# Performance work log

Measured on AMD Instinct MI355X. Metric: run time of the kernel, lower is better.

Reference implementation:

```python
import jax, jax.numpy as jnp
import numpy as np

CH = 256
GROUPS = 8
EPS = 1e-5


def setup_inputs() -> dict:
    key = jax.random.key(0)
    ks = jax.random.split(key, 12)
    b, c, h, w = 8, CH, 64, 64
    s = 0.02
    return {
        "x": jax.random.normal(ks[0], (b, c, h, w), dtype=jnp.float32),
        "gn_w": jnp.ones((c,), dtype=jnp.float32),
        "gn_b": jnp.zeros((c,), dtype=jnp.float32),
        "wq": jax.random.normal(ks[1], (c, c), dtype=jnp.float32) * s,
        "bq": jax.random.normal(ks[2], (c,), dtype=jnp.float32) * s,
        "wk": jax.random.normal(ks[3], (c, c), dtype=jnp.float32) * s,
        "bk": jax.random.normal(ks[4], (c,), dtype=jnp.float32) * s,
        "wv": jax.random.normal(ks[5], (c, c), dtype=jnp.float32) * s,
        "bv": jax.random.normal(ks[6], (c,), dtype=jnp.float32) * s,
        "wp": jax.random.normal(ks[7], (c, c), dtype=jnp.float32) * s,
        "bp": jax.random.normal(ks[8], (c,), dtype=jnp.float32) * s,
    }


def reference(x, gn_w, gn_b, wq, bq, wk, bk, wv, bv, wp, bp):
    b, c, h, w = x.shape
    n = h * w
    # GroupNorm(8, c): normalize over (c//g, h, w) per group, then affine per-channel
    xg = x.reshape(b, GROUPS, c // GROUPS, n)
    mu = xg.mean(axis=(2, 3), keepdims=True)
    var = xg.var(axis=(2, 3), keepdims=True)
    y = ((xg - mu) * jax.lax.rsqrt(var + EPS)).reshape(b, c, n)
    y = y * gn_w[None, :, None] + gn_b[None, :, None]
    # 1x1 convs == channel matmuls
    q = jnp.einsum('oc,bcn->bno', wq, y) + bq              # [b, n, c]
    k = jnp.einsum('oc,bcn->bon', wk, y) + bk[:, None]     # [b, c, n]
    v = jnp.einsum('oc,bcn->bno', wv, y) + bv              # [b, n, c]
    scale = 1.0 / jnp.sqrt(jnp.float32(c))
    attn = jax.nn.softmax(jnp.einsum('bnc,bcm->bnm', q, k) * scale, axis=-1)  # [b, n, n]
    out = jnp.einsum('bnm,bmc->bcn', attn, v)              # [b, c, n]
    proj = jnp.einsum('oc,bcn->bon', wp, out) + bp[:, None]
    return x + proj.reshape(b, c, h, w)
```

## Files before the change

### kernel.cpp

```cpp
#include <hip/hip_runtime.h>

typedef __attribute__((ext_vector_type(8))) short s16x8;
typedef __attribute__((ext_vector_type(4))) float f32x4;
typedef __attribute__((ext_vector_type(16))) float f32x16;
typedef __attribute__((ext_vector_type(4))) uint u32x4;
typedef __attribute__((ext_vector_type(2))) uint u32x2;
typedef __attribute__((ext_vector_type(2))) long s64x2;
typedef __attribute__((ext_vector_type(8))) int i32x8;
typedef unsigned char u8;

#define MFMA16(a, b, c) __builtin_amdgcn_mfma_f32_16x16x32_bf16((a), (b), (c), 0, 0, 0)
#define MFMAF8(a, b, c) __builtin_amdgcn_mfma_f32_32x32x16_fp8_fp8((a), (b), (c), 0, 0, 0)
#define MFMAMX(a, b, c) \
  __builtin_amdgcn_mfma_scale_f32_32x32x64_f8f6f4((a), (b), (c), 0, 0, 0, 0x7F7F7F7F, 0, 0x7F7F7F7F)

__device__ __forceinline__ ushort f2bf(float f) {
  uint u = __builtin_bit_cast(uint, f);
  u = (u + 0x7fffu + ((u >> 16) & 1u)) >> 16;
  return (ushort)u;
}
__device__ __forceinline__ float max3f(float a, float b, float c) {
  return fmaxf(fmaxf(a, b), c);
}

__global__ __launch_bounds__(256) void cvt_w_kernel(
    const float* __restrict__ s0, const float* __restrict__ s1,
    const float* __restrict__ s2, const float* __restrict__ s3,
    ushort* __restrict__ d0, ushort* __restrict__ d1,
    ushort* __restrict__ d2, ushort* __restrict__ d3,
    const float* __restrict__ bq, const float* __restrict__ bk,
    const float* __restrict__ bv, float* __restrict__ bcat) {
  int i = blockIdx.x * 256 + threadIdx.x;
  const float4* s[4] = {(const float4*)s0, (const float4*)s1, (const float4*)s2, (const float4*)s3};
  ushort* d[4] = {d0, d1, d2, d3};
#pragma unroll
  for (int m = 0; m < 4; ++m) {
    float4 v = s[m][i];
    uint lo = (uint)f2bf(v.x) | ((uint)f2bf(v.y) << 16);
    uint hi = (uint)f2bf(v.z) | ((uint)f2bf(v.w) << 16);
    *(uint2*)(d[m] + (size_t)i * 4) = make_uint2(lo, hi);
  }
  if (blockIdx.x == 0) {
    int t = threadIdx.x;
    bcat[t] = bq[t];
    bcat[256 + t] = bk[t];
    bcat[512 + t] = bv[t];
  }
}

__global__ __launch_bounds__(256) void gn_stats_kernel(
    const float* __restrict__ x, float2* __restrict__ partial) {
  int bid = blockIdx.x;
  int b = bid >> 6, g = (bid >> 3) & 7, sl = bid & 7;
  const float4* src = (const float4*)(x + ((size_t)b * 256 + g * 32) * 4096) + sl * 4096;
  float s = 0.f, ss = 0.f;
#pragma unroll 4
  for (int i = threadIdx.x; i < 4096; i += 256) {
    float4 v = src[i];
    s += v.x + v.y + v.z + v.w;
    ss += v.x * v.x + v.y * v.y + v.z * v.z + v.w * v.w;
  }
#pragma unroll
  for (int off = 32; off; off >>= 1) {
    s += __shfl_down(s, off);
    ss += __shfl_down(ss, off);
  }
  __shared__ float ps[4], pss[4];
  int w = threadIdx.x >> 6, lane = threadIdx.x & 63;
  if (lane == 0) { ps[w] = s; pss[w] = ss; }
  __syncthreads();
  if (threadIdx.x == 0) {
    float2 r;
    r.x = ps[0] + ps[1] + ps[2] + ps[3];
    r.y = pss[0] + pss[1] + pss[2] + pss[3];
    partial[bid] = r;
  }
}

__global__ __launch_bounds__(256) void gn_apply_kernel(
    const float* __restrict__ x, const float2* __restrict__ partial,
    const float* __restrict__ gw, const float* __restrict__ gb,
    ushort* __restrict__ y) {
  int bid = blockIdx.x;
  int b = bid >> 8;
  int rem = bid & 255;
  int ct = rem >> 6, nt = rem & 63;
  int t = threadIdx.x;
  __shared__ float xs[64][65];
  __shared__ float smu2[2], srs2[2];
  if (t < 2) {
    float S = 0.f, SS = 0.f;
#pragma unroll
    for (int i = 0; i < 8; ++i) {
      float2 p = partial[(b << 6) | ((2 * ct + t) << 3) | i];
      S += p.x;
      SS += p.y;
    }
    float mu = S * (1.f / 131072.f);
    float var = SS * (1.f / 131072.f) - mu * mu;
    smu2[t] = mu;
    srs2[t] = rsqrtf(var + 1e-5f);
  }
  const float* xb = x + ((size_t)b * 256 + ct * 64) * 4096 + nt * 64;
  {
    int r = t >> 2, q = t & 3;
    const float4* src = (const float4*)(xb + (size_t)r * 4096 + q * 16);
#pragma unroll
    for (int i = 0; i < 4; ++i) {
      float4 v = src[i];
      xs[r][q * 16 + i * 4 + 0] = v.x;
      xs[r][q * 16 + i * 4 + 1] = v.y;
      xs[r][q * 16 + i * 4 + 2] = v.z;
      xs[r][q * 16 + i * 4 + 3] = v.w;
    }
  }
  __syncthreads();
  {
    int nr = t >> 2, q = t & 3;
    int c0 = q * 16;
    ushort tmp[16];
#pragma unroll
    for (int i = 0; i < 16; ++i) {
      int ci = c0 + i;
      int ch = ct * 64 + ci;
      int gsel = ci >> 5;
      float sc = gw[ch] * srs2[gsel];
      float sh = gb[ch] - smu2[gsel] * sc;
      float v = xs[ci][nr] * sc + sh;
      tmp[i] = f2bf(v);
    }
    ushort* dst = y + ((size_t)b * 4096 + nt * 64 + nr) * 256 + ct * 64 + c0;
    uint p[8];
#pragma unroll
    for (int j = 0; j < 8; ++j) p[j] = (uint)tmp[2 * j] | ((uint)tmp[2 * j + 1] << 16);
    *(uint4*)dst = make_uint4(p[0], p[1], p[2], p[3]);
    *((uint4*)dst + 1) = make_uint4(p[4], p[5], p[6], p[7]);
  }
}

template <int MODE>
__global__ __launch_bounds__(256) void gemm_bt(
    const ushort* __restrict__ A, const ushort* __restrict__ B,
    size_t aB, size_t bB, int M, int N,
    const float* __restrict__ bias, const float* __restrict__ resid,
    size_t rB, void* __restrict__ Cout, size_t cB) {
  int mTiles = M >> 7;
  int tm = blockIdx.x % mTiles, tn = blockIdx.x / mTiles;
  const ushort* Ab = A + blockIdx.y * aB + (size_t)tm * 128 * 256;
  const ushort* Bb = B + blockIdx.y * bB + (size_t)tn * 128 * 256;

  __shared__ ushort As[2][8192];
  __shared__ ushort Bs[2][8192];

  int t = threadIdx.x, lane = t & 63, w = t >> 6;
  int wr = w >> 1, wc = w & 1, lq = lane & 15, lg = lane >> 4;

  f32x4 acc[4][4];
#pragma unroll
  for (int i = 0; i < 4; ++i)
#pragma unroll
    for (int j = 0; j < 4; ++j) acc[i][j] = f32x4{0.f, 0.f, 0.f, 0.f};

  auto stageT = [&](int kb, int db) {
#pragma unroll
    for (int i = 0; i < 4; ++i) {
      int bu = i * 256 + w * 64;
      int u = bu + lane;
      int row = u >> 3, c = u & 7;
      int cl = c ^ (row & 7);
      const ushort* sa = Ab + (size_t)row * 256 + kb * 64 + cl * 8;
      __builtin_amdgcn_global_load_lds(
          (const __attribute__((address_space(1))) uint*)sa,
          (__attribute__((address_space(3))) uint*)(&As[db][0] + bu * 8), 16, 0, 0);
      const ushort* sb = Bb + (size_t)row * 256 + kb * 64 + cl * 8;
      __builtin_amdgcn_global_load_lds(
          (const __attribute__((address_space(1))) uint*)sb,
          (__attribute__((address_space(3))) uint*)(&Bs[db][0] + bu * 8), 16, 0, 0);
    }
  };

  stageT(0, 0);

#pragma unroll 1
  for (int kb = 0; kb < 4; ++kb) {
    if (kb < 3) {
      stageT(kb + 1, (kb + 1) & 1);
      asm volatile("s_waitcnt vmcnt(8)" ::: "memory");
    } else {
      asm volatile("s_waitcnt vmcnt(0)" ::: "memory");
    }
    __builtin_amdgcn_s_barrier();
    const ushort* Abf = &As[kb & 1][0];
    const ushort* Bbf = &Bs[kb & 1][0];
#pragma unroll
    for (int ks = 0; ks < 2; ++ks) {
      s16x8 af[4], bf[4];
#pragma unroll
      for (int mt = 0; mt < 4; ++mt) {
        int row = wr * 64 + mt * 16 + lq;
        af[mt] = *(const s16x8*)&Abf[row * 64 + (((ks * 4 + lg) ^ (row & 7)) << 3)];
      }
#pragma unroll
      for (int nt = 0; nt < 4; ++nt) {
        int row = wc * 64 + nt * 16 + lq;
        bf[nt] = *(const s16x8*)&Bbf[row * 64 + (((ks * 4 + lg) ^ (row & 7)) << 3)];
      }
#pragma unroll
      for (int mt = 0; mt < 4; ++mt)
#pragma unroll
        for (int nt = 0; nt < 4; ++nt)
          acc[mt][nt] = MFMA16(af[mt], bf[nt], acc[mt][nt]);
    }
    asm volatile("" ::: "memory");
    __builtin_amdgcn_s_barrier();
    asm volatile("" ::: "memory");
  }

  int mBase = tm * 128 + wr * 64;
  int nBase = tn * 128 + wc * 64;
#pragma unroll
  for (int mt = 0; mt < 4; ++mt) {
#pragma unroll
    for (int nt = 0; nt < 4; ++nt) {
#pragma unroll
      for (int r = 0; r < 4; ++r) {
        int row = mBase + mt * 16 + lg * 4 + r;
        int col = nBase + nt * 16 + lq;
        float v = acc[mt][nt][r];
        if (MODE == 6) {
          v += bias[col];
          uint pk8 = (uint)__builtin_amdgcn_cvt_pk_fp8_f32(v, v, 0, false);
          u8* Cb = (u8*)Cout + blockIdx.y * cB;
          if (col < 512) {
            u8* C = Cb + ((col >= 256) ? 16777216 : 0);
            C[(size_t)row * 256 + (col & 255)] = (u8)(pk8 & 0xff);
          } else {
            int rr = row & 31;
            int pr = (row & ~31) |
                     ((rr & 7) | (((rr >> 4) & 1) << 3) | (((rr >> 3) & 1) << 4));
            u8* C = Cb + 33554432;
            C[(size_t)(col - 512) * 4096 + pr] = (u8)(pk8 & 0xff);
          }
        } else {
          v += bias[row];
          size_t idx = (size_t)row * N + col;
          float* C = (float*)Cout + blockIdx.y * cB;
          C[idx] = v + resid[blockIdx.y * rB + idx];
        }
      }
    }
  }
}

__global__ __launch_bounds__(256) void gemm_proj_kernel(
    const ushort* __restrict__ A, const ushort* __restrict__ P0,
    const ushort* __restrict__ P1, const float* __restrict__ mlb,
    const float* __restrict__ bias, const float* __restrict__ resid,
    float* __restrict__ Cout) {
  const size_t MAT = 4096 * 256;
  int tm = blockIdx.x & 1, tn = blockIdx.x >> 1;
  int bb = blockIdx.y;
  const ushort* Ab = A + (size_t)tm * 128 * 256;
  const ushort* P0b = P0 + (size_t)bb * MAT + (size_t)tn * 128 * 256;
  const ushort* P1b = P1 + (size_t)bb * MAT + (size_t)tn * 128 * 256;
  const int mlbase = bb * 4096 + tn * 128;

  __shared__ ushort As[2][8192];
  __shared__ ushort Bs[2][8192];

  int t = threadIdx.x, lane = t & 63, w = t >> 6;
  int wr = w >> 1, wc = w & 1, lq = lane & 15, lg = lane >> 4;

  f32x4 acc[4][4];
#pragma unroll
  for (int i = 0; i < 4; ++i)
#pragma unroll
    for (int j = 0; j < 4; ++j) acc[i][j] = f32x4{0.f, 0.f, 0.f, 0.f};

  u32x4 rb0[4], rb1[4];
  float rw0[4], rw1[4];

  auto issueA = [&](int kb, int db) {
#pragma unroll
    for (int i = 0; i < 4; ++i) {
      int bu = i * 256 + w * 64;
      int u = bu + lane;
      int row = u >> 3, c = u & 7;
      int cl = c ^ (row & 7);
      const ushort* sa = Ab + (size_t)row * 256 + kb * 64 + cl * 8;
      __builtin_amdgcn_global_load_lds(
          (const __attribute__((address_space(1))) uint*)sa,
          (__attribute__((address_space(3))) uint*)(&As[db][0] + bu * 8), 16, 0, 0);
    }
  };
  auto loadB = [&](int kb) {
#pragma unroll
    for (int i = 0; i < 4; ++i) {
      int bu = i * 256 + w * 64;
      int u = bu + lane;
      int row = u >> 3, c = u & 7;
      int cl = c ^ (row & 7);
      rb0[i] = *(const u32x4*)(P0b + (size_t)row * 256 + kb * 64 + cl * 8);
      rb1[i] = *(const u32x4*)(P1b + (size_t)row * 256 + kb * 64 + cl * 8);
      int gr = mlbase + row;
      float m0 = mlb[gr], m1 = mlb[32768 + gr];
      float l0 = mlb[65536 + gr], l1 = mlb[98304 + gr];
      float M = fmaxf(m0, m1);
      float e0 = __builtin_exp2f(m0 - M), e1 = __builtin_exp2f(m1 - M);
      float inv = 1.f / (l0 * e0 + l1 * e1);
      rw0[i] = e0 * inv;
      rw1[i] = e1 * inv;
    }
  };
  auto writeB = [&](int db) {
#pragma unroll
    for (int i = 0; i < 4; ++i) {
      int bu = i * 256 + w * 64;
      uint outw[4];
#pragma unroll
      for (int j = 0; j < 4; ++j) {
        float alo = __builtin_bit_cast(float, rb0[i][j] << 16);
        float ahi = __builtin_bit_cast(float, rb0[i][j] & 0xffff0000u);
        float blo = __builtin_bit_cast(float, rb1[i][j] << 16);
        float bhi = __builtin_bit_cast(float, rb1[i][j] & 0xffff0000u);
        float flo = alo * rw0[i] + blo * rw1[i];
        float fhi = ahi * rw0[i] + bhi * rw1[i];
        asm("v_cvt_pk_bf16_f32 %0, %1, %2" : "=v"(outw[j]) : "v"(flo), "v"(fhi));
      }
      u32x4 ov = {outw[0], outw[1], outw[2], outw[3]};
      *(u32x4*)&Bs[db][(size_t)(bu + lane) * 8] = ov;
    }
  };

  issueA(0, 0);
  loadB(0);
  writeB(0);
  asm volatile("s_waitcnt vmcnt(0) lgkmcnt(0)" ::: "memory");
  __builtin_amdgcn_s_barrier();

#pragma unroll
  for (int kb = 0; kb < 4; ++kb) {
    const int db = kb & 1;
    if (kb < 3) {
      issueA(kb + 1, db ^ 1);
      loadB(kb + 1);
    }
    const ushort* Abf = &As[db][0];
    const ushort* Bbf = &Bs[db][0];
#pragma unroll
    for (int ks = 0; ks < 2; ++ks) {
      s16x8 af[4], bf[4];
#pragma unroll
      for (int mt = 0; mt < 4; ++mt) {
        int row = wr * 64 + mt * 16 + lq;
        af[mt] = *(const s16x8*)&Abf[row * 64 + (((ks * 4 + lg) ^ (row & 7)) << 3)];
      }
#pragma unroll
      for (int nt = 0; nt < 4; ++nt) {
        int row = wc * 64 + nt * 16 + lq;
        bf[nt] = *(const s16x8*)&Bbf[row * 64 + (((ks * 4 + lg) ^ (row & 7)) << 3)];
      }
#pragma unroll
      for (int mt = 0; mt < 4; ++mt)
#pragma unroll
        for (int nt = 0; nt < 4; ++nt)
          acc[mt][nt] = MFMA16(af[mt], bf[nt], acc[mt][nt]);
    }
    if (kb < 3) writeB(db ^ 1);
    asm volatile("s_waitcnt vmcnt(0) lgkmcnt(0)" ::: "memory");
    __builtin_amdgcn_s_barrier();
  }

  int mBase = tm * 128 + wr * 64;
  int nBase = tn * 128 + wc * 64;
#pragma unroll
  for (int mt = 0; mt < 4; ++mt) {
#pragma unroll
    for (int nt = 0; nt < 4; ++nt) {
#pragma unroll
      for (int r = 0; r < 4; ++r) {
        int row = mBase + mt * 16 + lg * 4 + r;
        int col = nBase + nt * 16 + lq;
        size_t idx = (size_t)bb * MAT + (size_t)row * 4096 + col;
        Cout[idx] = acc[mt][nt][r] + bias[row] + resid[idx];
      }
    }
  }
}

__global__ __launch_bounds__(256, 2) void attn11_kernel(
    const u8* __restrict__ q, const u8* __restrict__ k,
    const u8* __restrict__ vT, ushort* __restrict__ pb0,
    ushort* __restrict__ pb1, float* __restrict__ mlbuf) {
  const int bb = blockIdx.x & 7;
  const int rem = blockIdx.x >> 3;
  const int qt = rem & 31;
  const int half = rem >> 5;
  const int t = threadIdx.x, w = t >> 6, lane = t & 63;
  const int lq = lane & 31, lh = lane >> 5;

  __shared__ u8 Lf[65536];

  const u8* kb = k + (size_t)bb * (4096 * 256);
  const u8* vb = vT + (size_t)bb * (4096 * 256);

  const int qrow = bb * 4096 + qt * 128 + w * 32 + lq;
  i32x8 qf8[4];
  {
    const u8* qp = q + (size_t)qrow * 256 + lh * 32;
#pragma unroll
    for (int ks = 0; ks < 4; ++ks) {
      u32x4 lo = *(const u32x4*)(qp + ks * 64);
      u32x4 hi = *(const u32x4*)(qp + ks * 64 + 16);
      qf8[ks] = i32x8{(int)lo[0], (int)lo[1], (int)lo[2], (int)lo[3],
                      (int)hi[0], (int)hi[1], (int)hi[2], (int)hi[3]};
    }
  }
  f32x16 oacc[8];
#pragma unroll
  for (int i = 0; i < 8; ++i) oacc[i] = (f32x16)(0.f);
  float mrun = -3e38f, lrun = 0.f;
  const float cs = 0.0625f * 1.44269504f;

  auto stage = [&](int it, int db) {
    const int ci = half * 64 + it;
    const u8* kcb = kb + (size_t)ci * (32 * 256);
    const u8* vcb = vb + (size_t)ci * 32;
    u8* base = Lf + db * 16384;
#pragma unroll
    for (int i = 0; i < 2; ++i) {
      int bu = w * 128 + i * 64;
      int Pu = bu + lane;
      {
        int Lu = Pu ^ ((Pu >> 4) & 7);
        const u8* ksrc = kcb + (Lu >> 4) * 256 + (Lu & 15) * 16;
        __builtin_amdgcn_global_load_lds(
            (const __attribute__((address_space(1))) uint*)ksrc,
            (__attribute__((address_space(3))) uint*)(base + bu * 16), 16, 0, 0);
      }
      {
        int Lu = Pu ^ ((Pu >> 3) & 7);
        const u8* vsrc = vcb + (size_t)(Lu >> 1) * 4096 + (Lu & 1) * 16;
        __builtin_amdgcn_global_load_lds(
            (const __attribute__((address_space(1))) uint*)vsrc,
            (__attribute__((address_space(3))) uint*)(base + 8192 + bu * 16), 16, 0, 0);
      }
    }
  };

  stage(0, 0);

#pragma unroll 1
  for (int j = 0; j < 64; ++j) {
    if (j < 63) {
      stage(j + 1, (j + 1) & 1);
      asm volatile("s_waitcnt vmcnt(4)" ::: "memory");
    } else {
      asm volatile("s_waitcnt vmcnt(0)" ::: "memory");
    }
    __builtin_amdgcn_s_barrier();

    const u8* Kbf = Lf + (j & 1) * 16384;
    const u8* Vbf = Kbf + 8192;

    __builtin_amdgcn_s_setprio(1);
    f32x16 sA = (f32x16)(0.f), sB = (f32x16)(0.f);
#pragma unroll
    for (int ks = 0; ks < 4; ++ks) {
      int u0 = (lq * 16 + ks * 4 + lh * 2) ^ (lq & 7);
      int u1 = (lq * 16 + ks * 4 + lh * 2 + 1) ^ (lq & 7);
      u32x4 k0 = *(const u32x4*)(Kbf + u0 * 16);
      u32x4 k1 = *(const u32x4*)(Kbf + u1 * 16);
      i32x8 kf = i32x8{(int)k0[0], (int)k0[1], (int)k0[2], (int)k0[3],
                       (int)k1[0], (int)k1[1], (int)k1[2], (int)k1[3]};
      if (ks & 1) sB = MFMAMX(kf, qf8[ks], sB);
      else        sA = MFMAMX(kf, qf8[ks], sA);
    }
    __builtin_amdgcn_s_setprio(0);
    float tv[16];
#pragma unroll
    for (int r = 0; r < 16; ++r) tv[r] = sA[r] + sB[r];
    float g0 = max3f(tv[0], tv[1], tv[2]);
    float g1 = max3f(tv[3], tv[4], tv[5]);
    float g2 = max3f(tv[6], tv[7], tv[8]);
    float g3 = max3f(tv[9], tv[10], tv[11]);
    float g4 = max3f(tv[12], tv[13], tv[14]);
    float pmax_t = max3f(max3f(g0, g1, tv[15]), fmaxf(g2, g3), g4);
    pmax_t = fmaxf(pmax_t, __shfl_xor(pmax_t, 32));
    float pmax = pmax_t * cs;
    if (!__all(pmax - mrun <= 8.f)) {
      float mnew = fmaxf(mrun, pmax);
      float alpha = __builtin_exp2f(mrun - mnew);
#pragma unroll
      for (int i = 0; i < 8; ++i) oacc[i] *= alpha;
      lrun *= alpha;
      mrun = mnew;
    }
    float nm = -mrun;
    float sv[16], psum = 0.f;
#pragma unroll
    for (int r = 0; r < 16; ++r) {
      sv[r] = __builtin_exp2f(__builtin_fmaf(tv[r], cs, nm));
      psum += sv[r];
    }
    psum += __shfl_xor(psum, 32);
    lrun += psum;
    uint Aw = (uint)__builtin_amdgcn_cvt_pk_fp8_f32(sv[0], sv[1], 0, false);
    Aw = (uint)__builtin_amdgcn_cvt_pk_fp8_f32(sv[2], sv[3], (int)Aw, true);
    uint Bw = (uint)__builtin_amdgcn_cvt_pk_fp8_f32(sv[4], sv[5], 0, false);
    Bw = (uint)__builtin_amdgcn_cvt_pk_fp8_f32(sv[6], sv[7], (int)Bw, true);
    uint Cw = (uint)__builtin_amdgcn_cvt_pk_fp8_f32(sv[8], sv[9], 0, false);
    Cw = (uint)__builtin_amdgcn_cvt_pk_fp8_f32(sv[10], sv[11], (int)Cw, true);
    uint Dw = (uint)__builtin_amdgcn_cvt_pk_fp8_f32(sv[12], sv[13], 0, false);
    Dw = (uint)__builtin_amdgcn_cvt_pk_fp8_f32(sv[14], sv[15], (int)Dw, true);
    asm("v_permlane32_swap_b32 %0, %1" : "+v"(Aw), "+v"(Bw));
    asm("v_permlane32_swap_b32 %0, %1" : "+v"(Cw), "+v"(Dw));
    long pf0 = __builtin_bit_cast(long, (u32x2){Aw, Bw});
    long pf1 = __builtin_bit_cast(long, (u32x2){Cw, Dw});
    __builtin_amdgcn_s_setprio(1);
#pragma unroll
    for (int db = 0; db < 8; ++db) {
      int L = (db * 32 + lq) * 2 + lh;
      int Pu = L ^ ((L >> 3) & 7);
      u32x4 vr = *(const u32x4*)(Vbf + Pu * 16);
      s64x2 vp = __builtin_bit_cast(s64x2, vr);
      oacc[db] = MFMAF8(vp[0], pf0, oacc[db]);
      oacc[db] = MFMAF8(vp[1], pf1, oacc[db]);
    }
    __builtin_amdgcn_s_setprio(0);
    asm volatile("" ::: "memory");
    __builtin_amdgcn_s_barrier();
    asm volatile("" ::: "memory");
  }

  {
    uint* wregu = (uint*)Lf + w * 4096;
#pragma unroll
    for (int db = 0; db < 8; ++db)
#pragma unroll
      for (int rp = 0; rp < 8; ++rp) {
        int r0 = rp * 2;
        int d0 = db * 32 + (r0 & 3) + 8 * (r0 >> 2) + 4 * lh;
        uint pk;
        asm("v_cvt_pk_bf16_f32 %0, %1, %2"
            : "=v"(pk) : "v"(oacc[db][r0]), "v"(oacc[db][r0 + 1]));
        int idx = lq * 128 + (d0 >> 1);
        wregu[idx ^ ((lq & 7) << 2)] = pk;
      }
    if (lh == 0) {
      int idx = half * 32768 + bb * 4096 + qt * 128 + w * 32 + lq;
      mlbuf[idx] = mrun;
      mlbuf[65536 + idx] = lrun;
    }
  }
  __syncthreads();
  {
    int r = t >> 1;
    int wv2 = r >> 5, lqr = r & 31;
    const uint* basep = (const uint*)Lf + wv2 * 4096;
    ushort* pbase = half ? pb1 : pb0;
    ushort* dstr = pbase + ((size_t)bb * 4096 + qt * 128 + r) * 256 + (t & 1) * 128;
#pragma unroll
    for (int jj = 0; jj < 16; ++jj) {
      int ui = lqr * 128 + (t & 1) * 64 + jj * 4;
      u32x4 v = *(const u32x4*)(basep + (ui ^ ((lqr & 7) << 2)));
      *(u32x4*)(dstr + jj * 8) = v;
    }
  }
}

extern "C" void kernel_launch(void* const* d_in, const int* in_sizes, int n_in,
                              void* d_out, int out_size, void* d_ws, size_t ws_size,
                              hipStream_t stream) {
  const float* x   = (const float*)d_in[0];
  const float* gnw = (const float*)d_in[1];
  const float* gnb = (const float*)d_in[2];
  const float* wq  = (const float*)d_in[3];
  const float* bq  = (const float*)d_in[4];
  const float* wk  = (const float*)d_in[5];
  const float* bk  = (const float*)d_in[6];
  const float* wv  = (const float*)d_in[7];
  const float* bv  = (const float*)d_in[8];
  const float* wp  = (const float*)d_in[9];
  const float* bp  = (const float*)d_in[10];

  const size_t SEQ = 4096, CH = 256;
  const size_t MAT = SEQ * CH;
  char* ws = (char*)d_ws;
  const size_t BUF = 8 * MAT * 2;
  ushort* y    = (ushort*)(ws + 0 * BUF);
  u8*     qb8  = (u8*)(ws + 1 * BUF);
  u8*     kb8  = (u8*)(ws + 2 * BUF);
  u8*     vtb8 = (u8*)(ws + 3 * BUF);
  ushort* pb1  = (ushort*)(ws + 4 * BUF);
  ushort* pb0  = y;
  ushort* wqb  = (ushort*)(ws + 5 * BUF);
  ushort* wkb  = wqb + 65536;
  ushort* wvb  = wkb + 65536;
  ushort* wpb  = wvb + 65536;
  float*  bcat   = (float*)(wpb + 65536);
  float2* partial = (float2*)(bcat + 768);
  float*  mlbuf  = (float*)(partial + 512);

  cvt_w_kernel<<<64, 256, 0, stream>>>(wq, wk, wv, wp, wqb, wkb, wvb, wpb,
                                       bq, bk, bv, bcat);
  gn_stats_kernel<<<512, 256, 0, stream>>>(x, partial);
  gn_apply_kernel<<<2048, 256, 0, stream>>>(x, partial, gnw, gnb, y);

  gemm_bt<6><<<dim3(192, 8), 256, 0, stream>>>(y, wqb, MAT, 0, 4096, 768, bcat,
                                               nullptr, 0, qb8, MAT);

  attn11_kernel<<<512, 256, 0, stream>>>(qb8, kb8, vtb8, pb0, pb1, mlbuf);

  gemm_proj_kernel<<<dim3(64, 8), 256, 0, stream>>>(wpb, pb0, pb1, mlbuf, bp,
                                                    x, (float*)d_out);
}
```

Baseline: 196.3 us.

## Switch QKV projection to FP8 MX MFMA with FP8 normalized activations

GroupNorm output and the Q/K/V weights are now stored as FP8 instead of bf16. The QKV projection becomes a single-stage kernel that loads the full K=256 tile into LDS once and uses the 32x32x64 f8f6f4 scaled MFMA instead of a double-buffered bf16 16x16x32 loop. This halves activation and weight bytes and the number of MFMA issues. The cost is lower precision for the projection inputs, and the kernel loses its load/compute overlap.

```diff
diff --git a/kernel.cpp b/kernel.cpp
--- a/kernel.cpp
+++ b/kernel.cpp
@@ -24,21 +24,25 @@
 }
 
 __global__ __launch_bounds__(256) void cvt_w_kernel(
-    const float* __restrict__ s0, const float* __restrict__ s1,
-    const float* __restrict__ s2, const float* __restrict__ s3,
-    ushort* __restrict__ d0, ushort* __restrict__ d1,
-    ushort* __restrict__ d2, ushort* __restrict__ d3,
+    const float* __restrict__ wq, const float* __restrict__ wk,
+    const float* __restrict__ wv, const float* __restrict__ wp,
+    u8* __restrict__ wcat8, ushort* __restrict__ wpb,
     const float* __restrict__ bq, const float* __restrict__ bk,
     const float* __restrict__ bv, float* __restrict__ bcat) {
   int i = blockIdx.x * 256 + threadIdx.x;
-  const float4* s[4] = {(const float4*)s0, (const float4*)s1, (const float4*)s2, (const float4*)s3};
-  ushort* d[4] = {d0, d1, d2, d3};
-#pragma unroll
-  for (int m = 0; m < 4; ++m) {
+  const float4* s[3] = {(const float4*)wq, (const float4*)wk, (const float4*)wv};
+#pragma unroll
+  for (int m = 0; m < 3; ++m) {
     float4 v = s[m][i];
+    uint u = (uint)__builtin_amdgcn_cvt_pk_fp8_f32(v.x, v.y, 0, false);
+    u = (uint)__builtin_amdgcn_cvt_pk_fp8_f32(v.z, v.w, (int)u, true);
+    ((uint*)wcat8)[m * 16384 + i] = u;
+  }
+  {
+    float4 v = ((const float4*)wp)[i];
     uint lo = (uint)f2bf(v.x) | ((uint)f2bf(v.y) << 16);
     uint hi = (uint)f2bf(v.z) | ((uint)f2bf(v.w) << 16);
-    *(uint2*)(d[m] + (size_t)i * 4) = make_uint2(lo, hi);
+    *(uint2*)(wpb + (size_t)i * 4) = make_uint2(lo, hi);
   }
   if (blockIdx.x == 0) {
     int t = threadIdx.x;
@@ -80,7 +84,7 @@
 __global__ __launch_bounds__(256) void gn_apply_kernel(
     const float* __restrict__ x, const float2* __restrict__ partial,
     const float* __restrict__ gw, const float* __restrict__ gb,
-    ushort* __restrict__ y) {
+    u8* __restrict__ y8) {
   int bid = blockIdx.x;
   int b = bid >> 8;
   int rem = bid & 255;
@@ -118,7 +122,7 @@
   {
     int nr = t >> 2, q = t & 3;
     int c0 = q * 16;
-    ushort tmp[16];
+    float vv[16];
 #pragma unroll
     for (int i = 0; i < 16; ++i) {
       int ci = c0 + i;
@@ -126,126 +130,107 @@
       int gsel = ci >> 5;
       float sc = gw[ch] * srs2[gsel];
       float sh = gb[ch] - smu2[gsel] * sc;
-      float v = xs[ci][nr] * sc + sh;
-      tmp[i] = f2bf(v);
-    }
-    ushort* dst = y + ((size_t)b * 4096 + nt * 64 + nr) * 256 + ct * 64 + c0;
-    uint p[8];
-#pragma unroll
-    for (int j = 0; j < 8; ++j) p[j] = (uint)tmp[2 * j] | ((uint)tmp[2 * j + 1] << 16);
-    *(uint4*)dst = make_uint4(p[0], p[1], p[2], p[3]);
-    *((uint4*)dst + 1) = make_uint4(p[4], p[5], p[6], p[7]);
-  }
-}
-
-template <int MODE>
-__global__ __launch_bounds__(256) void gemm_bt(
-    const ushort* __restrict__ A, const ushort* __restrict__ B,
-    size_t aB, size_t bB, int M, int N,
-    const float* __restrict__ bias, const float* __restrict__ resid,
-    size_t rB, void* __restrict__ Cout, size_t cB) {
-  int mTiles = M >> 7;
-  int tm = blockIdx.x % mTiles, tn = blockIdx.x / mTiles;
-  const ushort* Ab = A + blockIdx.y * aB + (size_t)tm * 128 * 256;
-  const ushort* Bb = B + blockIdx.y * bB + (size_t)tn * 128 * 256;
-
-  __shared__ ushort As[2][8192];
-  __shared__ ushort Bs[2][8192];
+      vv[i] = xs[ci][nr] * sc + sh;
+    }
+    uint pw[4];
+#pragma unroll
+    for (int j = 0; j < 4; ++j) {
+      uint u = (uint)__builtin_amdgcn_cvt_pk_fp8_f32(vv[4 * j], vv[4 * j + 1], 0, false);
+      u = (uint)__builtin_amdgcn_cvt_pk_fp8_f32(vv[4 * j + 2], vv[4 * j + 3], (int)u, true);
+      pw[j] = u;
+    }
+    u8* dst = y8 + ((size_t)(b * 4096 + nt * 64 + nr)) * 256 + ct * 64 + c0;
+    u32x4 ov = {pw[0], pw[1], pw[2], pw[3]};
+    *(u32x4*)dst = ov;
+  }
+}
+
+__global__ __launch_bounds__(256) void gemm_qkv_kernel(
+    const u8* __restrict__ A, const u8* __restrict__ B,
+    const float* __restrict__ bias, u8* __restrict__ Cq) {
+  int tm = blockIdx.x & 31, tn = blockIdx.x >> 5;
+  int bb = blockIdx.y;
+  const u8* Ab = A + (size_t)bb * (4096 * 256) + (size_t)tm * 128 * 256;
+  const u8* Bb = B + (size_t)tn * 128 * 256;
+
+  __shared__ u8 As[32768];
+  __shared__ u8 Bs[32768];
 
   int t = threadIdx.x, lane = t & 63, w = t >> 6;
-  int wr = w >> 1, wc = w & 1, lq = lane & 15, lg = lane >> 4;
-
-  f32x4 acc[4][4];
-#pragma unroll
-  for (int i = 0; i < 4; ++i)
-#pragma unroll
-    for (int j = 0; j < 4; ++j) acc[i][j] = f32x4{0.f, 0.f, 0.f, 0.f};
-
-  auto stageT = [&](int kb, int db) {
-#pragma unroll
-    for (int i = 0; i < 4; ++i) {
-      int bu = i * 256 + w * 64;
-      int u = bu + lane;
-      int row = u >> 3, c = u & 7;
-      int cl = c ^ (row & 7);
-      const ushort* sa = Ab + (size_t)row * 256 + kb * 64 + cl * 8;
-      __builtin_amdgcn_global_load_lds(
-          (const __attribute__((address_space(1))) uint*)sa,
-          (__attribute__((address_space(3))) uint*)(&As[db][0] + bu * 8), 16, 0, 0);
-      const ushort* sb = Bb + (size_t)row * 256 + kb * 64 + cl * 8;
-      __builtin_amdgcn_global_load_lds(
-          (const __attribute__((address_space(1))) uint*)sb,
-          (__attribute__((address_space(3))) uint*)(&Bs[db][0] + bu * 8), 16, 0, 0);
-    }
-  };
-
-  stageT(0, 0);
-
-#pragma unroll 1
-  for (int kb = 0; kb < 4; ++kb) {
-    if (kb < 3) {
-      stageT(kb + 1, (kb + 1) & 1);
-      asm volatile("s_waitcnt vmcnt(8)" ::: "memory");
-    } else {
-      asm volatile("s_waitcnt vmcnt(0)" ::: "memory");
-    }
-    __builtin_amdgcn_s_barrier();
-    const ushort* Abf = &As[kb & 1][0];
-    const ushort* Bbf = &Bs[kb & 1][0];
-#pragma unroll
-    for (int ks = 0; ks < 2; ++ks) {
-      s16x8 af[4], bf[4];
-#pragma unroll
-      for (int mt = 0; mt < 4; ++mt) {
-        int row = wr * 64 + mt * 16 + lq;
-        af[mt] = *(const s16x8*)&Abf[row * 64 + (((ks * 4 + lg) ^ (row & 7)) << 3)];
-      }
-#pragma unroll
-      for (int nt = 0; nt < 4; ++nt) {
-        int row = wc * 64 + nt * 16 + lq;
-        bf[nt] = *(const s16x8*)&Bbf[row * 64 + (((ks * 4 + lg) ^ (row & 7)) << 3)];
-      }
-#pragma unroll
-      for (int mt = 0; mt < 4; ++mt)
-#pragma unroll
-        for (int nt = 0; nt < 4; ++nt)
-          acc[mt][nt] = MFMA16(af[mt], bf[nt], acc[mt][nt]);
-    }
-    asm volatile("" ::: "memory");
-    __builtin_amdgcn_s_barrier();
-    asm volatile("" ::: "memory");
-  }
-
-  int mBase = tm * 128 + wr * 64;
-  int nBase = tn * 128 + wc * 64;
-#pragma unroll
-  for (int mt = 0; mt < 4; ++mt) {
-#pragma unroll
-    for (int nt = 0; nt < 4; ++nt) {
-#pragma unroll
-      for (int r = 0; r < 4; ++r) {
-        int row = mBase + mt * 16 + lg * 4 + r;
-        int col = nBase + nt * 16 + lq;
-        float v = acc[mt][nt][r];
-        if (MODE == 6) {
-          v += bias[col];
-          uint pk8 = (uint)__builtin_amdgcn_cvt_pk_fp8_f32(v, v, 0, false);
-          u8* Cb = (u8*)Cout + blockIdx.y * cB;
-          if (col < 512) {
-            u8* C = Cb + ((col >= 256) ? 16777216 : 0);
-            C[(size_t)row * 256 + (col & 255)] = (u8)(pk8 & 0xff);
-          } else {
-            int rr = row & 31;
-            int pr = (row & ~31) |
-                     ((rr & 7) | (((rr >> 4) & 1) << 3) | (((rr >> 3) & 1) << 4));
-            u8* C = Cb + 33554432;
-            C[(size_t)(col - 512) * 4096 + pr] = (u8)(pk8 & 0xff);
-          }
+  int wr = w >> 1, wc = w & 1, lq = lane & 31, lh = lane >> 5;
+
+  f32x16 acc[2][2];
+#pragma unroll
+  for (int i = 0; i < 2; ++i)
+#pragma unroll
+    for (int j = 0; j < 2; ++j) acc[i][j] = (f32x16)(0.f);
+
+#pragma unroll
+  for (int i = 0; i < 8; ++i) {
+    int bu = i * 256 + w * 64;
+    int Pu = bu + lane;
+    int Lu = Pu ^ ((Pu >> 4) & 7);
+    int off = (Lu >> 4) * 256 + (Lu & 15) * 16;
+    __builtin_amdgcn_global_load_lds(
+        (const __attribute__((address_space(1))) uint*)(Ab + off),
+        (__attribute__((address_space(3))) uint*)(As + bu * 16), 16, 0, 0);
+    __builtin_amdgcn_global_load_lds(
+        (const __attribute__((address_space(1))) uint*)(Bb + off),
+        (__attribute__((address_space(3))) uint*)(Bs + bu * 16), 16, 0, 0);
+  }
+  asm volatile("s_waitcnt vmcnt(0)" ::: "memory");
+  __builtin_amdgcn_s_barrier();
+
+#pragma unroll
+  for (int ks = 0; ks < 4; ++ks) {
+    i32x8 af[2], bf[2];
+#pragma unroll
+    for (int mt = 0; mt < 2; ++mt) {
+      int ra = wr * 64 + mt * 32 + lq;
+      int u0 = (ks * 4 + lh * 2) ^ (ra & 7);
+      int u1 = (ks * 4 + lh * 2 + 1) ^ (ra & 7);
+      u32x4 lo = *(const u32x4*)(As + ra * 256 + u0 * 16);
+      u32x4 hi = *(const u32x4*)(As + ra * 256 + u1 * 16);
+      af[mt] = i32x8{(int)lo[0], (int)lo[1], (int)lo[2], (int)lo[3],
+                     (int)hi[0], (int)hi[1], (int)hi[2], (int)hi[3]};
+    }
+#pragma unroll
+    for (int nt = 0; nt < 2; ++nt) {
+      int rb = wc * 64 + nt * 32 + lq;
+      int u0 = (ks * 4 + lh * 2) ^ (rb & 7);
+      int u1 = (ks * 4 + lh * 2 + 1) ^ (rb & 7);
+      u32x4 lo = *(const u32x4*)(Bs + rb * 256 + u0 * 16);
+      u32x4 hi = *(const u32x4*)(Bs + rb * 256 + u1 * 16);
+      bf[nt] = i32x8{(int)lo[0], (int)lo[1], (int)lo[2], (int)lo[3],
+                     (int)hi[0], (int)hi[1], (int)hi[2], (int)hi[3]};
+    }
+#pragma unroll
+    for (int mt = 0; mt < 2; ++mt)
+#pragma unroll
+      for (int nt = 0; nt < 2; ++nt)
+        acc[mt][nt] = MFMAMX(af[mt], bf[nt], acc[mt][nt]);
+  }
+
+  u8* Cb = Cq + (size_t)bb * (4096 * 256);
+#pragma unroll
+  for (int mt = 0; mt < 2; ++mt) {
+#pragma unroll
+    for (int nt = 0; nt < 2; ++nt) {
+#pragma unroll
+      for (int r = 0; r < 16; ++r) {
+        int row = tm * 128 + wr * 64 + mt * 32 + (r & 3) + 8 * (r >> 2) + 4 * lh;
+        int col = tn * 128 + wc * 64 + nt * 32 + lq;
+        float v = acc[mt][nt][r] + bias[col];
+        uint pk8 = (uint)__builtin_amdgcn_cvt_pk_fp8_f32(v, v, 0, false);
+        if (col < 512) {
+          u8* C = Cb + ((col >= 256) ? 16777216 : 0);
+          C[(size_t)row * 256 + (col & 255)] = (u8)(pk8 & 0xff);
         } else {
-          v += bias[row];
-          size_t idx = (size_t)row * N + col;
-          float* C = (float*)Cout + blockIdx.y * cB;
-          C[idx] = v + resid[blockIdx.y * rB + idx];
+          int rr = row & 31;
+          int pr = (row & ~31) |
+                   ((rr & 7) | (((rr >> 4) & 1) << 3) | (((rr >> 3) & 1) << 4));
+          u8* C = Cb + 33554432;
+          C[(size_t)(col - 512) * 4096 + pr] = (u8)(pk8 & 0xff);
         }
       }
     }
@@ -588,29 +573,25 @@
   const size_t MAT = SEQ * CH;
   char* ws = (char*)d_ws;
   const size_t BUF = 8 * MAT * 2;
-  ushort* y    = (ushort*)(ws + 0 * BUF);
+  u8*     y8   = (u8*)(ws + 0 * BUF);
   u8*     qb8  = (u8*)(ws + 1 * BUF);
-  u8*     kb8  = (u8*)(ws + 2 * BUF);
-  u8*     vtb8 = (u8*)(ws + 3 * BUF);
   ushort* pb1  = (ushort*)(ws + 4 * BUF);
-  ushort* pb0  = y;
-  ushort* wqb  = (ushort*)(ws + 5 * BUF);
-  ushort* wkb  = wqb + 65536;
-  ushort* wvb  = wkb + 65536;
-  ushort* wpb  = wvb + 65536;
-  float*  bcat   = (float*)(wpb + 65536);
+  ushort* pb0  = (ushort*)(ws + 0 * BUF);
+  ushort* wpb  = (ushort*)(ws + 5 * BUF);
+  u8*     wcat8 = (u8*)(wpb + 65536);
+  float*  bcat   = (float*)(wcat8 + 196608);
   float2* partial = (float2*)(bcat + 768);
   float*  mlbuf  = (float*)(partial + 512);
 
-  cvt_w_kernel<<<64, 256, 0, stream>>>(wq, wk, wv, wp, wqb, wkb, wvb, wpb,
+  cvt_w_kernel<<<64, 256, 0, stream>>>(wq, wk, wv, wp, wcat8, wpb,
                                        bq, bk, bv, bcat);
   gn_stats_kernel<<<512, 256, 0, stream>>>(x, partial);
-  gn_apply_kernel<<<2048, 256, 0, stream>>>(x, partial, gnw, gnb, y);
-
-  gemm_bt<6><<<dim3(192, 8), 256, 0, stream>>>(y, wqb, MAT, 0, 4096, 768, bcat,
-                                               nullptr, 0, qb8, MAT);
-
-  attn11_kernel<<<512, 256, 0, stream>>>(qb8, kb8, vtb8, pb0, pb1, mlbuf);
+  gn_apply_kernel<<<2048, 256, 0, stream>>>(x, partial, gnw, gnb, y8);
+
+  gemm_qkv_kernel<<<dim3(192, 8), 256, 0, stream>>>(y8, wcat8, bcat, qb8);
+
+  attn11_kernel<<<512, 256, 0, stream>>>(qb8, qb8 + 16777216, qb8 + 33554432,
+                                         pb0, pb1, mlbuf);
 
   gemm_proj_kernel<<<dim3(64, 8), 256, 0, stream>>>(wpb, pb0, pb1, mlbuf, bp,
                                                     x, (float*)d_out);
```

Result: faster. 188.9 us (-3.7%).
